# Kernel optimization log

Measured on AMD Instinct MI355X. Metric: run time of the kernel, lower is better.

## Reference

```python
import jax, jax.numpy as jnp
import numpy as np

FEATURE_MAPS = [38, 19, 10, 5, 3, 1]
NUM_ANCHORS = [4, 6, 6, 6, 4, 4]
SCALE_RANGE = (0.1, 0.9)
RATIO_RANGE = (0.5, 2.0)
BACKGROUND_ID = 0
EPS = 1e-6


def make_anchors():
    # Replicates AnchorManager._generate_anchors: for each level, loop i (rows -> cy),
    # j (cols -> cx), then zip(scales, ratios) anchor shapes. Returns [A, 4] cxcywh.
    all_a = []
    for size, na in zip(FEATURE_MAPS, NUM_ANCHORS):
        scales = np.linspace(SCALE_RANGE[0], SCALE_RANGE[1], na)
        ratios = np.linspace(RATIO_RANGE[0], RATIO_RANGE[1], na)
        rs = np.sqrt(ratios)
        w = scales * rs
        h = scales / rs
        c = (np.arange(size) + 0.5) / size
        cy_g, cx_g = np.meshgrid(c, c, indexing='ij')  # i -> cy, j -> cx
        centers = np.stack([cx_g.ravel(), cy_g.ravel()], axis=-1)  # [size*size, 2]
        wh = np.stack([w, h], axis=-1)  # [na, 2]
        a = np.concatenate([np.repeat(centers, na, axis=0), np.tile(wh, (size * size, 1))], axis=1)
        all_a.append(a)
    return np.concatenate(all_a).astype(np.float32)  # [8732, 4]


def _cxcywh_to_xyxy(b):
    return jnp.concatenate([b[..., :2] - b[..., 2:] * 0.5, b[..., :2] + b[..., 2:] * 0.5], axis=-1)


def _pairwise_iou(a, b):
    # a: [B, A, 4] xyxy, b: [B, N, 4] xyxy -> [B, A, N]
    lt = jnp.maximum(a[:, :, None, :2], b[:, None, :, :2])
    rb = jnp.minimum(a[:, :, None, 2:], b[:, None, :, 2:])
    wh = jnp.clip(rb - lt, 0.0)
    inter = wh[..., 0] * wh[..., 1]
    area_a = (a[..., 2] - a[..., 0]) * (a[..., 3] - a[..., 1])
    area_b = (b[..., 2] - b[..., 0]) * (b[..., 3] - b[..., 1])
    union = area_a[:, :, None] + area_b[:, None, :] - inter
    return inter / jnp.maximum(union, EPS)


def setup_inputs() -> dict:
    key = jax.random.key(0)
    k1, k2 = jax.random.split(key)
    B, N = 32, 100
    gt_boxes = jax.random.uniform(k1, (B, N, 4), dtype=jnp.float32)
    gt_labels = jax.random.randint(k2, (B, N), 0, 81, dtype=jnp.int32)
    mask = jnp.ones((B, N), dtype=bool)
    anchors = jnp.asarray(make_anchors())
    return {"gt_boxes": gt_boxes, "gt_labels": gt_labels, "mask": mask, "anchors": anchors}


def reference(gt_boxes, gt_labels, mask, anchors):
    B, N, _ = gt_boxes.shape
    A = anchors.shape[0]
    anc = jnp.broadcast_to(anchors, (B, A, 4))
    anc_xyxy = _cxcywh_to_xyxy(anc)
    ious = _pairwise_iou(anc_xyxy, gt_boxes)  # [B, A, N]

    best_gt_iou = ious.max(axis=-1)          # [B, A]
    best_gt_idx = ious.argmax(axis=-1)       # [B, A]
    best_anchor_idx = ious.argmax(axis=-2)   # [B, N]

    bidx = jnp.arange(B)[:, None]
    best_gt_idx = best_gt_idx.at[bidx, best_anchor_idx].set(jnp.broadcast_to(jnp.arange(N), (B, N)))
    best_gt_iou = best_gt_iou.at[bidx, best_anchor_idx].set(2.0)

    pos_mask = best_gt_iou > 0.5  # [B, A]

    matched_gtb = jnp.take_along_axis(gt_boxes, best_gt_idx[..., None], axis=1)  # [B, A, 4]
    matched_lab = jnp.take_along_axis(gt_labels, best_gt_idx, axis=1)           # [B, A]

    ex = (matched_gtb[..., 0] - anc[..., 0]) / anc[..., 2]
    ey = (matched_gtb[..., 1] - anc[..., 1]) / anc[..., 3]
    ew = jnp.log((matched_gtb[..., 2] + EPS) / (anc[..., 2] + EPS))
    eh = jnp.log((matched_gtb[..., 3] + EPS) / (anc[..., 3] + EPS))
    encoded = jnp.stack([ex, ey, ew, eh], axis=-1)  # [B, A, 4]

    encoded_labels = jnp.where(pos_mask, matched_lab, jnp.int32(BACKGROUND_ID))

    # Batches with no valid GT keep zeros / background (the `continue` branch)
    any_valid = mask.any(axis=-1)  # [B]
    encoded = jnp.where(any_valid[:, None, None], encoded, 0.0)
    encoded_labels = jnp.where(any_valid[:, None], encoded_labels, jnp.int32(BACKGROUND_ID))
    return encoded, encoded_labels, pos_mask
```

## Files before the change

kernel.cpp:

```cpp
#include <hip/hip_runtime.h>

#define A_ 8732
#define B_ 32
#define N_ 100
#define ABLK 35
#define GB_G 8
#define GMAX 13
#define G0 4
#define SPLIT 16
#define SLEN 546
#define EPSF 1e-6f



__global__ __launch_bounds__(256) void k_scan(
    const float* __restrict__ gt, const float* __restrict__ anchors,
    unsigned long long* __restrict__ partial,
    unsigned long long* __restrict__ wsplit) {
  int tid = threadIdx.x;
  int lane = tid & 63, wid = tid >> 6;
  int bid = blockIdx.x;
  int s = bid % SPLIT;
  int t = bid / SPLIT;
  int g0 = t % G0;
  int b = t / G0;

  __shared__ unsigned long long s_bal[2];
  __shared__ int s_slot[N_];
  __shared__ unsigned long long s_w[4][GB_G];

  bool v = false;
  if (tid < N_) {
    float4 myg = ((const float4*)gt)[b * N_ + tid];
    v = (myg.z > myg.x && myg.w > myg.y);
  }
  unsigned long long bal = __ballot(v);
  if (lane == 0 && wid < 2) s_bal[wid] = bal;
  __syncthreads();
  int c0 = __popcll(s_bal[0]);
  int c = c0 + __popcll(s_bal[1]);
  if (v) {
    int rank = __popcll(bal & ((1ull << lane) - 1)) + (wid ? c0 : 0);
    s_slot[rank] = tid;
  }
  __syncthreads();

  int s0 = s * SLEN;
  int send = (s0 + SLEN < A_) ? (s0 + SLEN) : A_;

  for (int g = g0; GB_G * g < c; g += G0) {
    float gx0[GB_G], gy0[GB_G], gx1[GB_G], gy1[GB_G], gar[GB_G];
    int gn[GB_G];
    bool live[GB_G];
#pragma unroll
    for (int j = 0; j < GB_G; j++) {
      int p = GB_G * g + j;
      live[j] = p < c;
      int nj = live[j] ? s_slot[p] : 0;
      gn[j] = nj;
      float4 gb = ((const float4*)gt)[b * N_ + nj];
      if (!live[j]) gb = make_float4(1.0f, 1.0f, 0.0f, 0.0f);
      gx0[j] = gb.x; gy0[j] = gb.y; gx1[j] = gb.z; gy1[j] = gb.w;
      gar[j] = (gb.z - gb.x) * (gb.w - gb.y);
    }
    unsigned long long wkey[GB_G];
#pragma unroll
    for (int j = 0; j < GB_G; j++)
      wkey[j] = (unsigned long long)(0xFFFFFFFFu - (unsigned)(s0 + tid));

    unsigned long long* prow = partial + ((size_t)b * GMAX + g) * A_;
    for (int a = s0 + tid; a < send; a += 256) {
      float4 an = ((const float4*)anchors)[a];
      float ax0 = an.x - an.z * 0.5f, ay0 = an.y - an.w * 0.5f;
      float ax1 = an.x + an.z * 0.5f, ay1 = an.y + an.w * 0.5f;
      float area_a = (ax1 - ax0) * (ay1 - ay0);
      unsigned long long pk = 0ull;
#pragma unroll
      for (int j = 0; j < GB_G; j++) {
        float lx = fmaxf(ax0, gx0[j]), ly = fmaxf(ay0, gy0[j]);
        float rx = fminf(ax1, gx1[j]), ry = fminf(ay1, gy1[j]);
        float w = fmaxf(rx - lx, 0.0f), h = fmaxf(ry - ly, 0.0f);
        float inter = w * h;
        if (inter > 0.0f) {
          float uni = area_a + gar[j] - inter;
          float iou = inter / fmaxf(uni, EPSF);
          unsigned long long hi =
              ((unsigned long long)__float_as_uint(iou)) << 32;
          unsigned long long kA =
              hi | (unsigned long long)(unsigned)(N_ - 1 - gn[j]);
          if (kA > pk) pk = kA;
          unsigned long long kB =
              hi | (unsigned long long)(0xFFFFFFFFu - (unsigned)a);
          if (kB > wkey[j]) wkey[j] = kB;
        }
      }
      prow[a] = pk;
    }

#pragma unroll
    for (int j = 0; j < GB_G; j++) {
      unsigned long long k = wkey[j];
#pragma unroll
      for (int off = 32; off; off >>= 1) {
        unsigned long long o = __shfl_xor(k, off, 64);
        if (o > k) k = o;
      }
      if (lane == 0) s_w[wid][j] = k;
    }
    __syncthreads();
    if (tid < GB_G) {
      int j = tid;
      if (GB_G * g + j < c) {
        unsigned long long k = s_w[0][j];
#pragma unroll
        for (int w2 = 1; w2 < 4; w2++)
          if (s_w[w2][j] > k) k = s_w[w2][j];
        wsplit[((size_t)b * SPLIT + s) * N_ + s_slot[GB_G * g + j]] = k;
      }
    }
    __syncthreads();
  }
}

__global__ __launch_bounds__(256) void k_finalize(
    const float* __restrict__ gt, const int* __restrict__ labels,
    const float* __restrict__ anchors, const unsigned char* __restrict__ mask,
    const unsigned long long* __restrict__ partial,
    const unsigned long long* __restrict__ wsplit, float* __restrict__ out) {
  int b = blockIdx.y;
  int a0 = blockIdx.x * 256;
  int tid = threadIdx.x;
  int lane = tid & 63, wid = tid >> 6;
  int a = a0 + tid;

  __shared__ int s_ov[256];
  __shared__ int s_any;
  __shared__ unsigned long long s_bal[2];

  bool v = false;
  if (tid < N_) {
    float4 gb = ((const float4*)gt)[b * N_ + tid];
    v = (gb.z > gb.x && gb.w > gb.y);
  }
  unsigned long long bal = __ballot(v);
  if (lane == 0 && wid < 2) s_bal[wid] = bal;
  if (tid == 0) s_any = 0;
  s_ov[tid] = -1;
  __syncthreads();
  int c = __popcll(s_bal[0]) + __popcll(s_bal[1]);

  if (tid < N_) {
    int aw = 0;
    if (v) {
      const unsigned long long* wp = wsplit + (size_t)b * SPLIT * N_ + tid;
      unsigned long long k = wp[0];
#pragma unroll
      for (int s2 = 1; s2 < SPLIT; s2++) {
        unsigned long long tk = wp[(size_t)s2 * N_];
        if (tk > k) k = tk;
      }
      aw = (int)(0xFFFFFFFFu - (unsigned)(k & 0xFFFFFFFFull));
    }
    if (aw >= a0 && aw < a0 + 256) atomicMax(&s_ov[aw - a0], tid);
  }
  if (tid < 25) {
    unsigned mv = ((const unsigned*)mask)[b * 25 + tid];
    if (mv) atomicOr(&s_any, 1);
  }
  __syncthreads();
  if (a >= A_) return;

  int G = (c + GB_G - 1) / GB_G;
  unsigned long long k = (unsigned long long)(unsigned)(N_ - 1);
  const unsigned long long* prow = partial + (size_t)b * GMAX * A_ + a;
  for (int g2 = 0; g2 < G; g2++) {
    unsigned long long t2 = prow[(size_t)g2 * A_];
    if (t2 > k) k = t2;
  }
  float iou = __uint_as_float((unsigned)(k >> 32));
  int gi = (N_ - 1) - (int)(k & 0xFFFFFFFFull);

  int ov = s_ov[tid];
  bool pos;
  if (ov >= 0) {
    gi = ov;
    pos = true;
  } else {
    pos = iou > 0.5f;
  }

  float4 an = ((const float4*)anchors)[a];
  const float* g = gt + (size_t)(b * N_ + gi) * 4;
  float gx = g[0], gy = g[1], gw = g[2], gh = g[3];

  float ex = (gx - an.x) / an.z;
  float ey = (gy - an.y) / an.w;
  float ew = logf((gw + EPSF) / (an.z + EPSF));
  float eh = logf((gh + EPSF) / (an.w + EPSF));
  int lab = pos ? labels[b * N_ + gi] : 0;

  if (!s_any) { ex = 0.0f; ey = 0.0f; ew = 0.0f; eh = 0.0f; lab = 0; }

  const long long BA = (long long)B_ * A_;
  ((float4*)out)[(size_t)b * A_ + a] = make_float4(ex, ey, ew, eh);
  out[4 * BA + (size_t)b * A_ + a] = (float)lab;
  out[5 * BA + (size_t)b * A_ + a] = pos ? 1.0f : 0.0f;
}

extern "C" void kernel_launch(void* const* d_in, const int* in_sizes, int n_in,
                              void* d_out, int out_size, void* d_ws,
                              size_t ws_size, hipStream_t stream) {
  const float* gt = (const float*)d_in[0];
  const int* labels = (const int*)d_in[1];
  const unsigned char* mask = (const unsigned char*)d_in[2];
  const float* anchors = (const float*)d_in[3];
  float* out = (float*)d_out;

  unsigned long long* partial = (unsigned long long*)d_ws;
  unsigned long long* wsplit = partial + (size_t)B_ * GMAX * A_;

  k_scan<<<B_ * G0 * SPLIT, 256, 0, stream>>>(gt, anchors, partial, wsplit);
  k_finalize<<<dim3(ABLK, B_), 256, 0, stream>>>(gt, labels, anchors, mask,
                                                 partial, wsplit, out);
}
```

Before: 83.29 us.

## Recompute per-anchor best IoU in finalize instead of storing partial keys

Result: slower. 86.53 us (+3.9%).

```diff
diff --git a/kernel.cpp b/kernel.cpp
--- a/kernel.cpp
+++ b/kernel.cpp
@@ -5,7 +5,6 @@
 #define N_ 100
 #define ABLK 35
 #define GB_G 8
-#define GMAX 13
 #define G0 4
 #define SPLIT 16
 #define SLEN 546
@@ -15,7 +14,6 @@
 
 __global__ __launch_bounds__(256) void k_scan(
     const float* __restrict__ gt, const float* __restrict__ anchors,
-    unsigned long long* __restrict__ partial,
     unsigned long long* __restrict__ wsplit) {
   int tid = threadIdx.x;
   int lane = tid & 63, wid = tid >> 6;
@@ -50,14 +48,12 @@
 
   for (int g = g0; GB_G * g < c; g += G0) {
     float gx0[GB_G], gy0[GB_G], gx1[GB_G], gy1[GB_G], gar[GB_G];
-    int gn[GB_G];
     bool live[GB_G];
 #pragma unroll
     for (int j = 0; j < GB_G; j++) {
       int p = GB_G * g + j;
       live[j] = p < c;
       int nj = live[j] ? s_slot[p] : 0;
-      gn[j] = nj;
       float4 gb = ((const float4*)gt)[b * N_ + nj];
       if (!live[j]) gb = make_float4(1.0f, 1.0f, 0.0f, 0.0f);
       gx0[j] = gb.x; gy0[j] = gb.y; gx1[j] = gb.z; gy1[j] = gb.w;
@@ -68,13 +64,11 @@
     for (int j = 0; j < GB_G; j++)
       wkey[j] = (unsigned long long)(0xFFFFFFFFu - (unsigned)(s0 + tid));
 
-    unsigned long long* prow = partial + ((size_t)b * GMAX + g) * A_;
     for (int a = s0 + tid; a < send; a += 256) {
       float4 an = ((const float4*)anchors)[a];
       float ax0 = an.x - an.z * 0.5f, ay0 = an.y - an.w * 0.5f;
       float ax1 = an.x + an.z * 0.5f, ay1 = an.y + an.w * 0.5f;
       float area_a = (ax1 - ax0) * (ay1 - ay0);
-      unsigned long long pk = 0ull;
 #pragma unroll
       for (int j = 0; j < GB_G; j++) {
         float lx = fmaxf(ax0, gx0[j]), ly = fmaxf(ay0, gy0[j]);
@@ -84,17 +78,12 @@
         if (inter > 0.0f) {
           float uni = area_a + gar[j] - inter;
           float iou = inter / fmaxf(uni, EPSF);
-          unsigned long long hi =
-              ((unsigned long long)__float_as_uint(iou)) << 32;
-          unsigned long long kA =
-              hi | (unsigned long long)(unsigned)(N_ - 1 - gn[j]);
-          if (kA > pk) pk = kA;
           unsigned long long kB =
-              hi | (unsigned long long)(0xFFFFFFFFu - (unsigned)a);
+              (((unsigned long long)__float_as_uint(iou)) << 32) |
+              (unsigned long long)(0xFFFFFFFFu - (unsigned)a);
           if (kB > wkey[j]) wkey[j] = kB;
         }
       }
-      prow[a] = pk;
     }
 
 #pragma unroll
@@ -125,7 +114,6 @@
 __global__ __launch_bounds__(256) void k_finalize(
     const float* __restrict__ gt, const int* __restrict__ labels,
     const float* __restrict__ anchors, const unsigned char* __restrict__ mask,
-    const unsigned long long* __restrict__ partial,
     const unsigned long long* __restrict__ wsplit, float* __restrict__ out) {
   int b = blockIdx.y;
   int a0 = blockIdx.x * 256;
@@ -136,18 +124,29 @@
   __shared__ int s_ov[256];
   __shared__ int s_any;
   __shared__ unsigned long long s_bal[2];
+  __shared__ float s_bx0[N_], s_by0[N_], s_bx1[N_], s_by1[N_], s_ar[N_];
+  __shared__ unsigned s_inv[N_];
 
   bool v = false;
+  float4 myg;
   if (tid < N_) {
-    float4 gb = ((const float4*)gt)[b * N_ + tid];
-    v = (gb.z > gb.x && gb.w > gb.y);
+    myg = ((const float4*)gt)[b * N_ + tid];
+    v = (myg.z > myg.x && myg.w > myg.y);
   }
   unsigned long long bal = __ballot(v);
   if (lane == 0 && wid < 2) s_bal[wid] = bal;
   if (tid == 0) s_any = 0;
   s_ov[tid] = -1;
   __syncthreads();
-  int c = __popcll(s_bal[0]) + __popcll(s_bal[1]);
+  int c0 = __popcll(s_bal[0]);
+  int c = c0 + __popcll(s_bal[1]);
+  if (v) {
+    int rank = __popcll(bal & ((1ull << lane) - 1)) + (wid ? c0 : 0);
+    s_bx0[rank] = myg.x; s_by0[rank] = myg.y;
+    s_bx1[rank] = myg.z; s_by1[rank] = myg.w;
+    s_ar[rank] = (myg.z - myg.x) * (myg.w - myg.y);
+    s_inv[rank] = (unsigned)(N_ - 1 - tid);
+  }
 
   if (tid < N_) {
     int aw = 0;
@@ -170,12 +169,25 @@
   __syncthreads();
   if (a >= A_) return;
 
-  int G = (c + GB_G - 1) / GB_G;
+  float4 an = ((const float4*)anchors)[a];
+  float ax0 = an.x - an.z * 0.5f, ay0 = an.y - an.w * 0.5f;
+  float ax1 = an.x + an.z * 0.5f, ay1 = an.y + an.w * 0.5f;
+  float area_a = (ax1 - ax0) * (ay1 - ay0);
+
   unsigned long long k = (unsigned long long)(unsigned)(N_ - 1);
-  const unsigned long long* prow = partial + (size_t)b * GMAX * A_ + a;
-  for (int g2 = 0; g2 < G; g2++) {
-    unsigned long long t2 = prow[(size_t)g2 * A_];
-    if (t2 > k) k = t2;
+  for (int j = 0; j < c; j++) {
+    float lx = fmaxf(ax0, s_bx0[j]), ly = fmaxf(ay0, s_by0[j]);
+    float rx = fminf(ax1, s_bx1[j]), ry = fminf(ay1, s_by1[j]);
+    float w = fmaxf(rx - lx, 0.0f), h = fmaxf(ry - ly, 0.0f);
+    float inter = w * h;
+    if (inter > 0.0f) {
+      float uni = area_a + s_ar[j] - inter;
+      float iou = inter / fmaxf(uni, EPSF);
+      unsigned long long kc =
+          (((unsigned long long)__float_as_uint(iou)) << 32) |
+          (unsigned long long)s_inv[j];
+      if (kc > k) k = kc;
+    }
   }
   float iou = __uint_as_float((unsigned)(k >> 32));
   int gi = (N_ - 1) - (int)(k & 0xFFFFFFFFull);
@@ -189,7 +201,6 @@
     pos = iou > 0.5f;
   }
 
-  float4 an = ((const float4*)anchors)[a];
   const float* g = gt + (size_t)(b * N_ + gi) * 4;
   float gx = g[0], gy = g[1], gw = g[2], gh = g[3];
 
@@ -216,10 +227,9 @@
   const float* anchors = (const float*)d_in[3];
   float* out = (float*)d_out;
 
-  unsigned long long* partial = (unsigned long long*)d_ws;
-  unsigned long long* wsplit = partial + (size_t)B_ * GMAX * A_;
-
-  k_scan<<<B_ * G0 * SPLIT, 256, 0, stream>>>(gt, anchors, partial, wsplit);
+  unsigned long long* wsplit = (unsigned long long*)d_ws;
+
+  k_scan<<<B_ * G0 * SPLIT, 256, 0, stream>>>(gt, anchors, wsplit);
   k_finalize<<<dim3(ABLK, B_), 256, 0, stream>>>(gt, labels, anchors, mask,
-                                                 partial, wsplit, out);
+                                                 wsplit, out);
 }
```
